# Optimization experiments

Hardware: AMD Instinct MI355X
Metric: run time of the kernel (lower is better)

The kernel has to match this reference:

```python
import jax, jax.numpy as jnp
import numpy as np

D_MODEL = 1024
N_HEADS = 16
HEAD_DIM = D_MODEL // N_HEADS
D_FF = 4096
EPS = 1e-5


def _layer_norm(x, gamma, beta):
    mu = jnp.mean(x, axis=-1, keepdims=True)
    var = jnp.var(x, axis=-1, keepdims=True)
    return (x - mu) * jax.lax.rsqrt(var + EPS) * gamma + beta


def setup_inputs() -> dict:
    key = jax.random.key(0)
    ks = jax.random.split(key, 16)
    B, T, S = 2, 2048, 2048
    s = 1.0 / np.sqrt(D_MODEL)
    inp = {
        "tgt": jax.random.normal(ks[0], (B, T, D_MODEL), jnp.float32),
        "memory": jax.random.normal(ks[1], (B, S, D_MODEL), jnp.float32),
        "wq": jax.random.normal(ks[2], (D_MODEL, D_MODEL), jnp.float32) * s,
        "bq": jnp.zeros((D_MODEL,), jnp.float32),
        "wk": jax.random.normal(ks[3], (D_MODEL, D_MODEL), jnp.float32) * s,
        "bk": jnp.zeros((D_MODEL,), jnp.float32),
        "wv": jax.random.normal(ks[4], (D_MODEL, D_MODEL), jnp.float32) * s,
        "bv": jnp.zeros((D_MODEL,), jnp.float32),
        "wo": jax.random.normal(ks[5], (D_MODEL, D_MODEL), jnp.float32) * s,
        "bo": jnp.zeros((D_MODEL,), jnp.float32),
        "w1": jax.random.normal(ks[6], (D_MODEL, D_FF), jnp.float32) * s,
        "b1": jnp.zeros((D_FF,), jnp.float32),
        "w2": jax.random.normal(ks[7], (D_FF, D_MODEL), jnp.float32) * (1.0 / np.sqrt(D_FF)),
        "b2": jnp.zeros((D_MODEL,), jnp.float32),
        "g1": jnp.ones((D_MODEL,), jnp.float32),
        "be1": jnp.zeros((D_MODEL,), jnp.float32),
        "g2": jnp.ones((D_MODEL,), jnp.float32),
        "be2": jnp.zeros((D_MODEL,), jnp.float32),
    }
    return inp


def reference(tgt, memory, wq, bq, wk, bk, wv, bv, wo, bo, w1, b1, w2, b2, g1, be1, g2, be2):
    B, T, _ = tgt.shape
    S = memory.shape[1]
    scale = HEAD_DIM ** -0.5
    # projections -> [B, H, L, Dh]
    Q = (tgt @ wq + bq).reshape(B, T, N_HEADS, HEAD_DIM).transpose(0, 2, 1, 3)
    K = (memory @ wk + bk).reshape(B, S, N_HEADS, HEAD_DIM).transpose(0, 2, 1, 3)
    V = (memory @ wv + bv).reshape(B, S, N_HEADS, HEAD_DIM).transpose(0, 2, 1, 3)
    scores = jnp.einsum("bhtd,bhsd->bhts", Q, K) * scale
    attn = jax.nn.softmax(scores, axis=-1)  # dropout=0 (eval)
    ctx = jnp.einsum("bhts,bhsd->bhtd", attn, V)
    ctx = ctx.transpose(0, 2, 1, 3).reshape(B, T, D_MODEL)
    attn_out = ctx @ wo + bo
    # post-norm residual blocks
    x = _layer_norm(tgt + attn_out, g1, be1)
    ff = jax.nn.relu(x @ w1 + b1) @ w2 + b2
    out = _layer_norm(x + ff, g2, be2)
    return out
```

## Files before the change

kernel.cpp:

```cpp
#include <hip/hip_runtime.h>


typedef unsigned short u16;
typedef __attribute__((ext_vector_type(8))) short bvec8;
typedef __attribute__((ext_vector_type(4))) float fvec4;

#define MFMA16(a, b, c) __builtin_amdgcn_mfma_f32_16x16x32_bf16((a), (b), (c), 0, 0, 0)

__device__ __forceinline__ u16 f2b(float f) {
  union { float f; unsigned u; } x; x.f = f;
  unsigned u = x.u;
  return (u16)((u + 0x7FFFu + ((u >> 16) & 1u)) >> 16);
}
__device__ __forceinline__ u16 f2b_t(float f) {
  union { float f; unsigned u; } x; x.f = f;
  return (u16)(x.u >> 16);
}
__device__ __forceinline__ void gl_lds16(const u16* g, u16* lds) {
  __builtin_amdgcn_global_load_lds(
      (const __attribute__((address_space(1))) void*)g,
      (__attribute__((address_space(3))) void*)lds, 16, 0, 0);
}

__global__ __launch_bounds__(256) void k_tobf(const float* __restrict__ in,
                                              u16* __restrict__ out, int n4) {
  int i = blockIdx.x * 256 + threadIdx.x;
  if (i >= n4) return;
  float4 v = ((const float4*)in)[i];
  ushort4 o;
  o.x = f2b(v.x); o.y = f2b(v.y); o.z = f2b(v.z); o.w = f2b(v.w);
  ((ushort4*)out)[i] = o;
}

__global__ __launch_bounds__(256) void k_wt(const float* __restrict__ W,
                                            u16* __restrict__ WT, int K, int N) {
  __shared__ float t[32][33];
  int tx = threadIdx.x & 31, ty = threadIdx.x >> 5;
  int n0 = blockIdx.x * 32, k0 = blockIdx.y * 32;
#pragma unroll
  for (int i = 0; i < 4; i++)
    t[ty + i * 8][tx] = W[(size_t)(k0 + ty + i * 8) * N + n0 + tx];
  __syncthreads();
#pragma unroll
  for (int i = 0; i < 4; i++)
    WT[(size_t)(n0 + ty + i * 8) * K + k0 + tx] = f2b(t[tx][ty + i * 8]);
}

__global__ __launch_bounds__(256) void k_vt(const u16* __restrict__ V,
                                            u16* __restrict__ Vt) {
  __shared__ u16 t[32][33];
  int tx = threadIdx.x & 31, ty = threadIdx.x >> 5;
  int s0 = blockIdx.x * 32, d0 = blockIdx.y * 32, bh = blockIdx.z;
  int b = bh >> 4, h = bh & 15;
#pragma unroll
  for (int i = 0; i < 4; i++)
    t[ty + i * 8][tx] = V[(size_t)(b * 2048 + s0 + ty + i * 8) * 1024 + h * 64 + d0 + tx];
  __syncthreads();
#pragma unroll
  for (int i = 0; i < 4; i++)
    Vt[((size_t)bh * 64 + d0 + ty + i * 8) * 2048 + s0 + tx] = t[tx][ty + i * 8];
}

template <int TM, int TN>
__global__ __launch_bounds__(256, TM == 64 ? 4 : 3) void k_gemm(
    const u16* __restrict__ A, const u16* __restrict__ BT,
    const float* __restrict__ bias, const float* __restrict__ bias2,
    const float* __restrict__ resid, float* __restrict__ outF,
    u16* __restrict__ outB, u16* __restrict__ outB2,
    int M, int N, int Kstride, int Klen, float scale, int flags) {
  constexpr int WM = TM / 2, WN = TN / 2;
  constexpr int MI = WM / 16, NI = WN / 16;
  constexpr int NCALL = (TM + TN) / 64;
  __shared__ u16 S[(TM + TN) * 32];
  const int tid = threadIdx.x, w = tid >> 6, lane = tid & 63;
  const int q = lane >> 4, l = lane & 15;
  const int m0 = blockIdx.y * TM, n0 = blockIdx.x * TN;
  const int kbeg = blockIdx.z * Klen;
  const int wm = (w >> 1) * WM, wn = (w & 1) * WN;
  const int srow = lane >> 2, sgrp = lane & 3;
  const int gcol = ((sgrp + (srow >> 1)) & 3) * 8;
  const int rpos = ((q + 4 - ((l >> 1) & 3)) & 3) * 8;
  const u16* gp[NCALL];
  u16* lp[NCALL];
#pragma unroll
  for (int c = 0; c < NCALL; c++) {
    int r0 = (w * NCALL + c) * 16;
    gp[c] = (r0 < TM) ? A + (size_t)(m0 + r0 + srow) * Kstride + kbeg + gcol
                      : BT + (size_t)(n0 + r0 - TM + srow) * Kstride + kbeg + gcol;
    lp[c] = &S[r0 * 32];
  }
  fvec4 acc[MI][NI] = {};
#pragma unroll 1
  for (int k0 = 0; k0 < Klen; k0 += 32) {
#pragma unroll
    for (int c = 0; c < NCALL; c++) gl_lds16(gp[c] + k0, lp[c]);
    __syncthreads();
    bvec8 af[MI], bf[NI];
#pragma unroll
    for (int i = 0; i < MI; i++)
      af[i] = *(const bvec8*)&S[(wm + 16 * i + l) * 32 + rpos];
#pragma unroll
    for (int j = 0; j < NI; j++)
      bf[j] = *(const bvec8*)&S[(TM + wn + 16 * j + l) * 32 + rpos];
#pragma unroll
    for (int i = 0; i < MI; i++)
#pragma unroll
      for (int j = 0; j < NI; j++)
        acc[i][j] = MFMA16(af[i], bf[j], acc[i][j]);
    __syncthreads();
  }
  if (flags & 16) {
    float* po = outF + (size_t)blockIdx.z * M * N;
#pragma unroll
    for (int mi = 0; mi < MI; mi++)
#pragma unroll
      for (int ni = 0; ni < NI; ni++) {
        int row = m0 + wm + mi * 16 + q * 4;
        int col = n0 + wn + ni * 16 + l;
#pragma unroll
        for (int r = 0; r < 4; r++)
          po[(size_t)(row + r) * N + col] = acc[mi][ni][r];
      }
    return;
  }
  const int On = outB2 ? 1024 : N;
#pragma unroll
  for (int mi = 0; mi < MI; mi++)
#pragma unroll
    for (int ni = 0; ni < NI; ni++) {
      int row = m0 + wm + mi * 16 + q * 4;
      int col = n0 + wn + ni * 16 + l;
      const float* bs = bias;
      u16* ob = outB;
      float sc = scale;
      int oc = col;
      if (outB2 && col >= 1024) { bs = bias2; ob = outB2; sc = 1.0f; oc = col - 1024; }
      float bv = bs[oc];
#pragma unroll
      for (int r = 0; r < 4; r++) {
        float v = (acc[mi][ni][r] + bv) * sc;
        if (flags & 1) v = fmaxf(v, 0.0f);
        size_t idx = (size_t)(row + r) * On + oc;
        if (flags & 8) v += resid[idx];
        if (flags & 2) ob[idx] = f2b(v);
        if (flags & 4) outF[idx] = v;
      }
    }
}

__global__ __launch_bounds__(256, 4) void k_attn(
    const u16* __restrict__ Q, const u16* __restrict__ Kb,
    const u16* __restrict__ Vt, float* __restrict__ opart,
    float* __restrict__ lpart) {
  __shared__ u16 Ks[64 * 64];
  __shared__ u16 Vs[64 * 64];
  __shared__ u16 Ps[4][2][16 * 72];
  const int tid = threadIdx.x, w = tid >> 6, lane = tid & 63;
  const int q = lane >> 4, l = lane & 15;
  const int blk = blockIdx.x;
  const int bh = blk >> 4, tb = blk & 15;
  const int b = bh >> 4, h = bh & 15;
  const int t0 = tb * 128 + w * 32;
  const int sbeg = blockIdx.y * 1024;
  float* op = opart + (size_t)blockIdx.y * 4096 * 1024;
  float* lp = lpart + (size_t)blockIdx.y * 4096 * 16;
  const u16* Qp = Q + (size_t)(b * 2048 + t0) * 1024 + h * 64;
  const u16* Kp = Kb + (size_t)(b * 2048) * 1024 + h * 64;
  const u16* Vp = Vt + (size_t)bh * 64 * 2048;
  const int rowin = lane >> 3, grp = lane & 7;
  const int gcol = ((grp + rowin) & 7) * 8;
  const int kc0 = ((q + 8 - (l & 7)) & 7) * 8;
  const int kc1 = ((q + 12 - (l & 7)) & 7) * 8;
  bvec8 aQ[2][2];
#pragma unroll
  for (int ti = 0; ti < 2; ti++)
#pragma unroll
    for (int kh = 0; kh < 2; kh++)
      aQ[ti][kh] = *(const bvec8*)&Qp[(size_t)(ti * 16 + l) * 1024 + kh * 32 + q * 8];
  fvec4 o[2][4] = {};
  float ls[2][4] = {};
#pragma unroll 1
  for (int s0 = sbeg; s0 < sbeg + 1024; s0 += 64) {
    gl_lds16(Kp + (size_t)(s0 + w * 8 + rowin) * 1024 + gcol, &Ks[(w * 8) * 64]);
    gl_lds16(Kp + (size_t)(s0 + 32 + w * 8 + rowin) * 1024 + gcol, &Ks[(32 + w * 8) * 64]);
    gl_lds16(Vp + (size_t)(w * 8 + rowin) * 2048 + s0 + gcol, &Vs[(w * 8) * 64]);
    gl_lds16(Vp + (size_t)(32 + w * 8 + rowin) * 2048 + s0 + gcol, &Vs[(32 + w * 8) * 64]);
    __syncthreads();
    fvec4 sc[2][4];
#pragma unroll
    for (int ti = 0; ti < 2; ti++)
#pragma unroll
      for (int ss = 0; ss < 4; ss++) sc[ti][ss] = (fvec4){0.f, 0.f, 0.f, 0.f};
#pragma unroll
    for (int ss = 0; ss < 4; ss++) {
      const int ro = (ss * 16 + l) * 64;
      bvec8 kf0 = *(const bvec8*)&Ks[ro + kc0];
      bvec8 kf1 = *(const bvec8*)&Ks[ro + kc1];
#pragma unroll
      for (int ti = 0; ti < 2; ti++) {
        sc[ti][ss] = MFMA16(aQ[ti][0], kf0, sc[ti][ss]);
        sc[ti][ss] = MFMA16(aQ[ti][1], kf1, sc[ti][ss]);
      }
    }
#pragma unroll
    for (int ti = 0; ti < 2; ti++)
#pragma unroll
      for (int ss = 0; ss < 4; ss++)
#pragma unroll
        for (int r = 0; r < 4; r++) {
          float p = __expf(sc[ti][ss][r]);
          ls[ti][r] += p;
          Ps[w][ti][(q * 4 + r) * 72 + ss * 16 + l] = f2b_t(p);
        }
    asm volatile("s_waitcnt lgkmcnt(0)" ::: "memory");
    bvec8 bV[4][2];
#pragma unroll
    for (int dt = 0; dt < 4; dt++) {
      const int ro = (dt * 16 + l) * 64;
      bV[dt][0] = *(const bvec8*)&Vs[ro + kc0];
      bV[dt][1] = *(const bvec8*)&Vs[ro + kc1];
    }
#pragma unroll
    for (int ti = 0; ti < 2; ti++) {
      bvec8 aP0 = *(const bvec8*)&Ps[w][ti][l * 72 + q * 8];
      bvec8 aP1 = *(const bvec8*)&Ps[w][ti][l * 72 + 32 + q * 8];
#pragma unroll
      for (int dt = 0; dt < 4; dt++) {
        o[ti][dt] = MFMA16(aP0, bV[dt][0], o[ti][dt]);
        o[ti][dt] = MFMA16(aP1, bV[dt][1], o[ti][dt]);
      }
    }
    __syncthreads();
  }
#pragma unroll
  for (int ti = 0; ti < 2; ti++)
#pragma unroll
    for (int r = 0; r < 4; r++) {
      float s = ls[ti][r];
      s += __shfl_xor(s, 1, 64);
      s += __shfl_xor(s, 2, 64);
      s += __shfl_xor(s, 4, 64);
      s += __shfl_xor(s, 8, 64);
      int trow = b * 2048 + t0 + ti * 16 + q * 4 + r;
      if (l == 0) lp[trow * 16 + h] = s;
#pragma unroll
      for (int dt = 0; dt < 4; dt++)
        op[(size_t)trow * 1024 + h * 64 + dt * 16 + l] = o[ti][dt][r];
    }
}

__global__ __launch_bounds__(256) void k_actx(const float* __restrict__ opart,
                                              const float* __restrict__ lpart,
                                              u16* __restrict__ ctx) {
  int row = blockIdx.x, c0 = threadIdx.x * 4;
  int h = c0 >> 6;
  float lsum = lpart[row * 16 + h] + lpart[4096 * 16 + row * 16 + h];
  float inv = 1.0f / lsum;
  float4 a = *(const float4*)&opart[(size_t)row * 1024 + c0];
  float4 b = *(const float4*)&opart[(size_t)4096 * 1024 + (size_t)row * 1024 + c0];
  ushort4 o;
  o.x = f2b((a.x + b.x) * inv);
  o.y = f2b((a.y + b.y) * inv);
  o.z = f2b((a.z + b.z) * inv);
  o.w = f2b((a.w + b.w) * inv);
  *(ushort4*)&ctx[(size_t)row * 1024 + c0] = o;
}

__global__ __launch_bounds__(256) void k_lnp(
    const float* __restrict__ p0, const float* __restrict__ p1,
    const float* __restrict__ bias, const float* __restrict__ resid,
    const float* __restrict__ g, const float* __restrict__ be,
    float* __restrict__ xf, u16* __restrict__ xb) {
  __shared__ float sm[8];
  int row = blockIdx.x, tid = threadIdx.x;
  size_t base = (size_t)row * 1024;
  float v[4], s = 0.f, ss = 0.f;
#pragma unroll
  for (int j = 0; j < 4; j++) {
    int c = tid + j * 256;
    v[j] = p0[base + c] + p1[base + c] + bias[c] + resid[base + c];
    s += v[j]; ss += v[j] * v[j];
  }
#pragma unroll
  for (int off = 32; off; off >>= 1) {
    s += __shfl_down(s, off, 64);
    ss += __shfl_down(ss, off, 64);
  }
  int w = tid >> 6;
  if ((tid & 63) == 0) { sm[w] = s; sm[4 + w] = ss; }
  __syncthreads();
  float S = sm[0] + sm[1] + sm[2] + sm[3];
  float SS = sm[4] + sm[5] + sm[6] + sm[7];
  float mean = S * (1.0f / 1024.0f);
  float var = SS * (1.0f / 1024.0f) - mean * mean;
  float rstd = rsqrtf(var + 1e-5f);
#pragma unroll
  for (int j = 0; j < 4; j++) {
    int c = tid + j * 256;
    float o = (v[j] - mean) * rstd * g[c] + be[c];
    xf[base + c] = o;
    if (xb) xb[base + c] = f2b(o);
  }
}

extern "C" void kernel_launch(void* const* d_in, const int* in_sizes, int n_in,
                              void* d_out, int out_size, void* d_ws, size_t ws_size,
                              hipStream_t stream) {
  (void)in_sizes; (void)n_in; (void)out_size; (void)ws_size;
  const float* tgt = (const float*)d_in[0];
  const float* mem = (const float*)d_in[1];
  const float* wq  = (const float*)d_in[2];
  const float* bq  = (const float*)d_in[3];
  const float* wk  = (const float*)d_in[4];
  const float* bk  = (const float*)d_in[5];
  const float* wv  = (const float*)d_in[6];
  const float* bv  = (const float*)d_in[7];
  const float* wo  = (const float*)d_in[8];
  const float* bo  = (const float*)d_in[9];
  const float* w1  = (const float*)d_in[10];
  const float* b1  = (const float*)d_in[11];
  const float* w2  = (const float*)d_in[12];
  const float* b2  = (const float*)d_in[13];
  const float* g1  = (const float*)d_in[14];
  const float* be1 = (const float*)d_in[15];
  const float* g2  = (const float*)d_in[16];
  const float* be2 = (const float*)d_in[17];
  float* out = (float*)d_out;

  char* ws = (char*)d_ws;
  size_t off = 0;
  auto take = [&](size_t bytes) { char* p = ws + off; off += bytes; return p; };
  const size_t MB = 1024 * 1024;
  u16* tgt_b = (u16*)take(8 * MB);
  u16* mem_b = (u16*)take(8 * MB);
  u16* wqT   = (u16*)take(2 * MB);
  u16* wkvT  = (u16*)take(4 * MB);
  u16* woT   = (u16*)take(2 * MB);
  u16* w1T   = (u16*)take(8 * MB);
  u16* w2T   = (u16*)take(8 * MB);
  u16* Qb    = (u16*)take(8 * MB);
  u16* Kb    = (u16*)take(8 * MB);
  u16* Vb    = (u16*)take(8 * MB);
  u16* Vtb   = (u16*)take(8 * MB);
  u16* ctx   = (u16*)take(8 * MB);
  float* opart = (float*)take(32 * MB);
  float* lpart = (float*)take(1 * MB);
  float* opj   = (float*)take(32 * MB);
  float* xf  = (float*)take(16 * MB);
  u16* xb    = (u16*)take(8 * MB);
  u16* hbuf  = Qb;
  float* fp2 = opart;

  k_tobf<<<4096, 256, 0, stream>>>(tgt, tgt_b, 4096 * 1024 / 4);
  k_tobf<<<4096, 256, 0, stream>>>(mem, mem_b, 4096 * 1024 / 4);
  k_wt<<<dim3(32, 32), 256, 0, stream>>>(wq, wqT, 1024, 1024);
  k_wt<<<dim3(32, 32), 256, 0, stream>>>(wk, wkvT, 1024, 1024);
  k_wt<<<dim3(32, 32), 256, 0, stream>>>(wv, wkvT + 1024 * 1024, 1024, 1024);
  k_wt<<<dim3(32, 32), 256, 0, stream>>>(wo, woT, 1024, 1024);
  k_wt<<<dim3(128, 32), 256, 0, stream>>>(w1, w1T, 1024, 4096);
  k_wt<<<dim3(32, 128), 256, 0, stream>>>(w2, w2T, 4096, 1024);
  k_gemm<64, 128><<<dim3(8, 64), 256, 0, stream>>>(
      tgt_b, wqT, bq, nullptr, nullptr, nullptr, Qb, nullptr,
      4096, 1024, 1024, 1024, 0.125f, 2);
  k_gemm<128, 128><<<dim3(16, 32), 256, 0, stream>>>(
      mem_b, wkvT, bk, bv, nullptr, nullptr, Kb, Vb,
      4096, 2048, 1024, 1024, 1.0f, 2);
  k_vt<<<dim3(64, 2, 32), 256, 0, stream>>>(Vb, Vtb);
  k_attn<<<dim3(512, 2), 256, 0, stream>>>(Qb, Kb, Vtb, opart, lpart);
  k_actx<<<4096, 256, 0, stream>>>(opart, lpart, ctx);
  k_gemm<64, 128><<<dim3(8, 64, 2), 256, 0, stream>>>(
      ctx, woT, nullptr, nullptr, nullptr, opj, nullptr, nullptr,
      4096, 1024, 1024, 512, 1.0f, 16);
  k_lnp<<<4096, 256, 0, stream>>>(opj, opj + 4096 * 1024, bo, tgt, g1, be1, xf, xb);
  k_gemm<128, 128><<<dim3(32, 32), 256, 0, stream>>>(
      xb, w1T, b1, nullptr, nullptr, nullptr, hbuf, nullptr,
      4096, 4096, 1024, 1024, 1.0f, 1 | 2);
  k_gemm<64, 128><<<dim3(8, 64, 2), 256, 0, stream>>>(
      hbuf, w2T, nullptr, nullptr, nullptr, fp2, nullptr, nullptr,
      4096, 1024, 4096, 2048, 1.0f, 16);
  k_lnp<<<4096, 256, 0, stream>>>(fp2, fp2 + 4096 * 1024, b2, xf, g2, be2, out, nullptr);
}
```

Measured before the change: 424.5 us.

## Batch prep kernels, shrink GEMM tiles, and use 4-way split-K for FF2

Merges the two fp32-to-bf16 conversions into one launch and the six weight-transpose launches into one indexed launch, removing per-launch overhead. Switches the KV and FF1 GEMMs from 128x128 to 64x128 tiles to get more blocks across the CUs. Splits FF2 along K four ways instead of two, and generalizes the layernorm-epilogue kernel to sum a variable number of partials. For that it reorders the workspace so the partial-sum buffer spans two adjacent 32MB regions. This buys more parallelism at the cost of extra fp32 partial traffic and smaller-tile reuse.

```diff
diff --git a/kernel.cpp b/kernel.cpp
--- a/kernel.cpp
+++ b/kernel.cpp
@@ -22,21 +22,43 @@
       (__attribute__((address_space(3))) void*)lds, 16, 0, 0);
 }
 
-__global__ __launch_bounds__(256) void k_tobf(const float* __restrict__ in,
-                                              u16* __restrict__ out, int n4) {
-  int i = blockIdx.x * 256 + threadIdx.x;
-  if (i >= n4) return;
+__global__ __launch_bounds__(256) void k_prep(const float* __restrict__ tgt,
+                                              const float* __restrict__ mem,
+                                              u16* __restrict__ tgt_b,
+                                              u16* __restrict__ mem_b) {
+  int bx = blockIdx.x;
+  const float* in = (bx < 4096) ? tgt : mem;
+  u16* out = (bx < 4096) ? tgt_b : mem_b;
+  int i = (bx & 4095) * 256 + threadIdx.x;
   float4 v = ((const float4*)in)[i];
   ushort4 o;
   o.x = f2b(v.x); o.y = f2b(v.y); o.z = f2b(v.z); o.w = f2b(v.w);
   ((ushort4*)out)[i] = o;
 }
 
-__global__ __launch_bounds__(256) void k_wt(const float* __restrict__ W,
-                                            u16* __restrict__ WT, int K, int N) {
+__global__ __launch_bounds__(256) void k_wtb(
+    const float* __restrict__ wq, const float* __restrict__ wk,
+    const float* __restrict__ wv, const float* __restrict__ wo,
+    const float* __restrict__ w1, const float* __restrict__ w2,
+    u16* __restrict__ wqT, u16* __restrict__ wkvT, u16* __restrict__ woT,
+    u16* __restrict__ w1T, u16* __restrict__ w2T) {
   __shared__ float t[32][33];
+  int b = blockIdx.x;
+  const float* W; u16* WT; int K, N, bx, by;
+  if (b < 4096) {
+    int m = b >> 10, tt = b & 1023;
+    bx = tt & 31; by = tt >> 5; K = 1024; N = 1024;
+    W = (m == 0) ? wq : (m == 1) ? wk : (m == 2) ? wv : wo;
+    WT = (m == 0) ? wqT : (m == 1) ? wkvT : (m == 2) ? wkvT + 1024 * 1024 : woT;
+  } else if (b < 8192) {
+    int tt = b - 4096; bx = tt & 127; by = tt >> 7; K = 1024; N = 4096;
+    W = w1; WT = w1T;
+  } else {
+    int tt = b - 8192; bx = tt & 31; by = tt >> 5; K = 4096; N = 1024;
+    W = w2; WT = w2T;
+  }
   int tx = threadIdx.x & 31, ty = threadIdx.x >> 5;
-  int n0 = blockIdx.x * 32, k0 = blockIdx.y * 32;
+  int n0 = bx * 32, k0 = by * 32;
 #pragma unroll
   for (int i = 0; i < 4; i++)
     t[ty + i * 8][tx] = W[(size_t)(k0 + ty + i * 8) * N + n0 + tx];
@@ -267,19 +289,22 @@
 }
 
 __global__ __launch_bounds__(256) void k_lnp(
-    const float* __restrict__ p0, const float* __restrict__ p1,
+    const float* __restrict__ parts, int nparts,
     const float* __restrict__ bias, const float* __restrict__ resid,
     const float* __restrict__ g, const float* __restrict__ be,
     float* __restrict__ xf, u16* __restrict__ xb) {
   __shared__ float sm[8];
   int row = blockIdx.x, tid = threadIdx.x;
   size_t base = (size_t)row * 1024;
+  const size_t pstride = (size_t)4096 * 1024;
   float v[4], s = 0.f, ss = 0.f;
 #pragma unroll
   for (int j = 0; j < 4; j++) {
     int c = tid + j * 256;
-    v[j] = p0[base + c] + p1[base + c] + bias[c] + resid[base + c];
-    s += v[j]; ss += v[j] * v[j];
+    float acc = bias[c] + resid[base + c];
+    for (int z = 0; z < nparts; z++) acc += parts[z * pstride + base + c];
+    v[j] = acc;
+    s += acc; ss += acc * acc;
   }
 #pragma unroll
   for (int off = 32; off; off >>= 1) {
@@ -344,25 +369,20 @@
   u16* Vtb   = (u16*)take(8 * MB);
   u16* ctx   = (u16*)take(8 * MB);
   float* opart = (float*)take(32 * MB);
+  float* opj   = (float*)take(32 * MB);
   float* lpart = (float*)take(1 * MB);
-  float* opj   = (float*)take(32 * MB);
   float* xf  = (float*)take(16 * MB);
   u16* xb    = (u16*)take(8 * MB);
   u16* hbuf  = Qb;
   float* fp2 = opart;
 
-  k_tobf<<<4096, 256, 0, stream>>>(tgt, tgt_b, 4096 * 1024 / 4);
-  k_tobf<<<4096, 256, 0, stream>>>(mem, mem_b, 4096 * 1024 / 4);
-  k_wt<<<dim3(32, 32), 256, 0, stream>>>(wq, wqT, 1024, 1024);
-  k_wt<<<dim3(32, 32), 256, 0, stream>>>(wk, wkvT, 1024, 1024);
-  k_wt<<<dim3(32, 32), 256, 0, stream>>>(wv, wkvT + 1024 * 1024, 1024, 1024);
-  k_wt<<<dim3(32, 32), 256, 0, stream>>>(wo, woT, 1024, 1024);
-  k_wt<<<dim3(128, 32), 256, 0, stream>>>(w1, w1T, 1024, 4096);
-  k_wt<<<dim3(32, 128), 256, 0, stream>>>(w2, w2T, 4096, 1024);
+  k_prep<<<8192, 256, 0, stream>>>(tgt, mem, tgt_b, mem_b);
+  k_wtb<<<12288, 256, 0, stream>>>(wq, wk, wv, wo, w1, w2,
+                                   wqT, wkvT, woT, w1T, w2T);
   k_gemm<64, 128><<<dim3(8, 64), 256, 0, stream>>>(
       tgt_b, wqT, bq, nullptr, nullptr, nullptr, Qb, nullptr,
       4096, 1024, 1024, 1024, 0.125f, 2);
-  k_gemm<128, 128><<<dim3(16, 32), 256, 0, stream>>>(
+  k_gemm<64, 128><<<dim3(16, 64), 256, 0, stream>>>(
       mem_b, wkvT, bk, bv, nullptr, nullptr, Kb, Vb,
       4096, 2048, 1024, 1024, 1.0f, 2);
   k_vt<<<dim3(64, 2, 32), 256, 0, stream>>>(Vb, Vtb);
@@ -371,12 +391,12 @@
   k_gemm<64, 128><<<dim3(8, 64, 2), 256, 0, stream>>>(
       ctx, woT, nullptr, nullptr, nullptr, opj, nullptr, nullptr,
       4096, 1024, 1024, 512, 1.0f, 16);
-  k_lnp<<<4096, 256, 0, stream>>>(opj, opj + 4096 * 1024, bo, tgt, g1, be1, xf, xb);
-  k_gemm<128, 128><<<dim3(32, 32), 256, 0, stream>>>(
+  k_lnp<<<4096, 256, 0, stream>>>(opj, 2, bo, tgt, g1, be1, xf, xb);
+  k_gemm<64, 128><<<dim3(32, 64), 256, 0, stream>>>(
       xb, w1T, b1, nullptr, nullptr, nullptr, hbuf, nullptr,
       4096, 4096, 1024, 1024, 1.0f, 1 | 2);
-  k_gemm<64, 128><<<dim3(8, 64, 2), 256, 0, stream>>>(
+  k_gemm<64, 128><<<dim3(8, 64, 4), 256, 0, stream>>>(
       hbuf, w2T, nullptr, nullptr, nullptr, fp2, nullptr, nullptr,
-      4096, 1024, 4096, 2048, 1.0f, 16);
-  k_lnp<<<4096, 256, 0, stream>>>(fp2, fp2 + 4096 * 1024, b2, xf, g2, be2, out, nullptr);
-}
+      4096, 1024, 4096, 1024, 1.0f, 16);
+  k_lnp<<<4096, 256, 0, stream>>>(fp2, 4, b2, xf, g2, be2, out, nullptr);
+}
```

Measured after the change: 447.0 us. 5.3% more time.
